# Kernel tuning notes

Measured on AMD Instinct MI355X. Metric: run time of the kernel, lower is better.

The kernel has to match this reference:

```python
import jax, jax.numpy as jnp
import numpy as np

B, T, I = 256, 1024, 64
P, E, NOUT = 256, 128, 64
K = 2
TEMP = 8.0
LN_EPS = 1e-5


def setup_inputs() -> dict:
    key = jax.random.key(0)
    ks = jax.random.split(key, 10)
    lim_in = 1.0 / np.sqrt(I)
    lim_e = 1.0 / np.sqrt(E)
    return {
        "x": jax.random.normal(ks[0], (B, T, I), dtype=jnp.float32),
        "pointer_init": jax.random.uniform(ks[1], (B,), dtype=jnp.float32) * P,
        "W_in": jax.random.uniform(ks[2], (E, I), minval=-lim_in, maxval=lim_in),
        "b_in": jax.random.uniform(ks[3], (E,), minval=-lim_in, maxval=lim_in),
        "ln_w": jnp.ones((E,), jnp.float32),
        "ln_b": jnp.zeros((E,), jnp.float32),
        "jump_dest": jax.random.uniform(ks[4], (P,), dtype=jnp.float32) * P,
        "Wg": jax.random.uniform(ks[5], (1, E), minval=-lim_e, maxval=lim_e),
        "bg": jax.random.uniform(ks[6], (1,), minval=-lim_e, maxval=lim_e),
        "context_strength": jnp.float32(0.2),
        "Wo": jax.random.uniform(ks[7], (NOUT, E), minval=-lim_e, maxval=lim_e),
        "bo": jax.random.uniform(ks[8], (NOUT,), minval=-lim_e, maxval=lim_e),
    }


def _layer_norm(h, w, b):
    mu = jnp.mean(h, axis=-1, keepdims=True)
    var = jnp.mean((h - mu) ** 2, axis=-1, keepdims=True)
    return (h - mu) * jax.lax.rsqrt(var + LN_EPS) * w + b


def reference(x, pointer_init, W_in, b_in, ln_w, ln_b, jump_dest, Wg, bg, context_strength, Wo, bo):
    Bsz = x.shape[0]
    nP = jump_dest.shape[0]
    offsets = jnp.arange(-K, K + 1, dtype=jnp.int32)  # [5]
    batch_idx = jnp.arange(Bsz)[:, None]               # [B,1]
    ctx_scale = jax.nn.sigmoid(context_strength)
    half = nP / 2.0

    def step(carry, x_t):
        mem, hid, ptr = carry                          # [B,P,E], [B,E], [B]
        emb = jnp.tanh(x_t @ W_in.T + b_in)            # [B,E]
        base = jnp.clip(jnp.floor(ptr).astype(jnp.int32), 0, nP - 1)
        idx = jnp.mod(base[:, None] + offsets[None, :], nP)  # [B,5]
        delta = jnp.mod(idx.astype(x_t.dtype) - ptr[:, None] + half, nP) - half
        w = jax.nn.softmax(-(delta ** 2) / TEMP, axis=1)     # [B,5]
        nbh = jnp.take_along_axis(mem, idx[:, :, None], axis=1)  # [B,5,E]
        ctx = jnp.sum(w[:, :, None] * nbh, axis=1)               # [B,E]
        su = jnp.tanh(emb + ctx_scale * ctx + hid)               # [B,E]
        hid_new = _layer_norm(su, ln_w, ln_b)
        mem_new = mem.at[batch_idx, idx].add(w[:, :, None] * su[:, None, :])
        cur = jnp.clip(ptr.astype(jnp.int32), 0, nP - 1)
        jt = jump_dest[cur]                                      # [B]
        jl = (su @ Wg.T + bg)[:, 0]                              # [B]
        probs = jax.nn.sigmoid(jl)
        sj = (probs > 0.5).astype(x_t.dtype) - jax.lax.stop_gradient(probs) + probs
        walk = jnp.mod(ptr + 1.0, nP)
        ptr_new = jnp.where(sj > 0.5, jt, walk)
        return (mem_new, hid_new, ptr_new), None

    mem0 = jnp.zeros((Bsz, nP, W_in.shape[0]), x.dtype)
    hid0 = jnp.zeros((Bsz, W_in.shape[0]), x.dtype)
    (mem, hid, ptr), _ = jax.lax.scan(step, (mem0, hid0, pointer_init), jnp.swapaxes(x, 0, 1))
    logits = hid @ Wo.T + bo
    return logits
```

## Files before the change

kernel.cpp:

```cpp
#include <hip/hip_runtime.h>
#include <math.h>

#define Bn    256
#define Tn    1024
#define In    64
#define Pn    256
#define En    128
#define NOUTn 64
#define LN_EPS 1e-5f

#define C1f 0.3606737602222409f
#define K1f 0.8824969025845955f
#define K2f 0.6065306597126334f

typedef float f32x2 __attribute__((ext_vector_type(2)));

__device__ __forceinline__ float tanh_fast(float x) {
    float e = __builtin_amdgcn_exp2f(x * 2.88539008177793f);
    return 1.0f - 2.0f * __builtin_amdgcn_rcpf(e + 1.0f);
}
__device__ __forceinline__ f32x2 tanh2(f32x2 x) {
    f32x2 e;
    e[0] = __builtin_amdgcn_exp2f(x[0] * 2.88539008177793f);
    e[1] = __builtin_amdgcn_exp2f(x[1] * 2.88539008177793f);
    f32x2 r;
    r[0] = __builtin_amdgcn_rcpf(e[0] + 1.0f);
    r[1] = __builtin_amdgcn_rcpf(e[1] + 1.0f);
    return 1.0f - 2.0f * r;
}

template<int CTRL, int RMASK>
__device__ __forceinline__ float dpp_add(float x) {
    return x + __int_as_float(__builtin_amdgcn_update_dpp(
        0, __float_as_int(x), CTRL, RMASK, 0xF, false));
}
__device__ __forceinline__ void wave_sum64_x3(float& x, float& y, float& z) {
#define LVL(C, R) x = dpp_add<C, R>(x); y = dpp_add<C, R>(y); z = dpp_add<C, R>(z);
    LVL(0x111, 0xF)
    LVL(0x112, 0xF)
    LVL(0x114, 0xF)
    LVL(0x118, 0xF)
    LVL(0x142, 0xA)
    LVL(0x143, 0xC)
#undef LVL
    x = __int_as_float(__builtin_amdgcn_readlane(__float_as_int(x), 63));
    y = __int_as_float(__builtin_amdgcn_readlane(__float_as_int(y), 63));
    z = __int_as_float(__builtin_amdgcn_readlane(__float_as_int(z), 63));
}

#define STAGE_FLOATS (3 * 16 * En)
#define LDSF_FLOATS  (Pn * En + Pn + STAGE_FLOATS)
#define LDSF_BYTES   (LDSF_FLOATS * 4)

__global__ __launch_bounds__(192, 1)
void fused2_kernel(const float* __restrict__ x,
                   const float* __restrict__ pointer_init,
                   const float* __restrict__ W_in, const float* __restrict__ b_in,
                   const float* __restrict__ ln_w, const float* __restrict__ ln_b,
                   const float* __restrict__ jump_dest,
                   const float* __restrict__ Wg,  const float* __restrict__ bg,
                   const float* __restrict__ cs_ptr,
                   const float* __restrict__ Wo,  const float* __restrict__ bo,
                   float* __restrict__ out) {
    extern __shared__ float lds[];
    float* mem = lds;
    float* jd  = lds + Pn * En;
    float* stg = lds + Pn * En + Pn;

    const int b   = blockIdx.x;
    const int tid = threadIdx.x;

    if (tid >= 64) {
        const int p    = tid - 64;
        const int tq   = p >> 5;
        const int eidx = p & 31;
        float be[4];
        #pragma unroll
        for (int j = 0; j < 4; ++j) be[j] = b_in[eidx + 32 * j];
        const float* xb = x + (size_t)b * Tn * In;

#define PRODUCE(K, BUF) {                                                     \
    const int t0 = (K) * 16 + tq * 4;                                         \
    const float4* xr = (const float4*)(xb + t0 * In);      \
    float acc[4][4];                                                          \
    _Pragma("unroll")                                                         \
    for (int tt = 0; tt < 4; ++tt)                                            \
        _Pragma("unroll")                                                     \
        for (int j = 0; j < 4; ++j) acc[tt][j] = 0.f;                         \
    _Pragma("unroll")                                                         \
    for (int i4 = 0; i4 < 16; ++i4) {                                         \
        float4 xv[4];                                                         \
        _Pragma("unroll")                                                     \
        for (int tt = 0; tt < 4; ++tt) xv[tt] = xr[tt * 16 + i4];             \
        float4 wf[4];                                                         \
        _Pragma("unroll")                                                     \
        for (int j = 0; j < 4; ++j)                                           \
            wf[j] = *(const float4*)(W_in + (eidx + 32 * j) * In + i4 * 4);   \
        _Pragma("unroll")                                                     \
        for (int tt = 0; tt < 4; ++tt)                                        \
            _Pragma("unroll")                                                 \
            for (int j = 0; j < 4; ++j) {                                     \
                acc[tt][j] += xv[tt].x * wf[j].x;                             \
                acc[tt][j] += xv[tt].y * wf[j].y;                             \
                acc[tt][j] += xv[tt].z * wf[j].z;                             \
                acc[tt][j] += xv[tt].w * wf[j].w;                             \
            }                                                                 \
    }                                                                         \
    float* sg = stg + (BUF) * 2048 + tq * 512;                                \
    _Pragma("unroll")                                                         \
    for (int j = 0; j < 4; ++j) {                                             \
        float4 o;                                                             \
        o.x = tanh_fast(acc[0][j] + be[j]);                                   \
        o.y = tanh_fast(acc[1][j] + be[j]);                                   \
        o.z = tanh_fast(acc[2][j] + be[j]);                                   \
        o.w = tanh_fast(acc[3][j] + be[j]);                                   \
        *(float4*)(sg + (eidx + 32 * j) * 4) = o;                             \
    }                                                                         \
}
        PRODUCE(0, 0)
        PRODUCE(1, 1)
        __syncthreads();
        int buf = 2;
        for (int k = 0; k < 64; ++k) {
            if (k + 2 < 64) {
                PRODUCE(k + 2, buf)
                buf = (buf == 2) ? 0 : buf + 1;
            }
            __syncthreads();
        }
#undef PRODUCE
        __syncthreads();
        return;
    }

    const int l = tid;

    float4* m4 = (float4*)mem;
    for (int i = l; i < Pn * En / 4; i += 64) m4[i] = make_float4(0.f, 0.f, 0.f, 0.f);
    for (int i = l; i < Pn; i += 64) jd[i] = jump_dest[i];

    const f32x2 lnw = {ln_w[l], ln_w[l + 64]};
    const f32x2 lnb = {ln_b[l], ln_b[l + 64]};
    const f32x2 wg  = {Wg[l],   Wg[l + 64]};
    const float bgs = bg[0];
    const float cs  = 1.0f / (1.0f + expf(-cs_ptr[0]));
    f32x2 hid = {0.f, 0.f};

    float* myb = mem + 2 * l;

    float jl      = 1.0f;
    float jt_cur  = pointer_init[b];
    float ptrW    = 0.f;
    int   baseW   = 0;
    float jtW_pre = 0.f;
    float z0 = 0.f, z1 = 0.f, z2 = 1.f, z3 = 0.f, z4 = 0.f, inv = 1.f;
    f32x2 wnb0 = {0,0}, wnb1 = {0,0}, wnb2 = {0,0}, wnb3 = {0,0}, wnb4 = {0,0};
    float *wp0 = myb, *wp1 = myb, *wp2 = myb, *wp3 = myb, *wp4 = myb;

    __syncthreads();

    const float* sa0 = stg + 4 * l;
    float4 A0 = *(const float4*)sa0;
    float4 A1 = *(const float4*)(sa0 + 256);

#define SSTEP(EC0, EC1) {                                                      \
    float ptr; int base;                                                       \
    f32x2 nb0, nb1, nb2, nb3, nb4;                                             \
    float *p0, *p1, *p2, *p3, *p4;                                             \
    float jt_nxt;                                                              \
    if (__builtin_amdgcn_readfirstlane(__float_as_int(jl)) > 0) {              \
                                     \
        ptr  = jt_cur;                                                         \
        base = (int)ptr; base = base > 255 ? 255 : base;                       \
        p0 = mem + (((base + 254) & 255) << 7) + 2 * l;                        \
        p1 = mem + (((base + 255) & 255) << 7) + 2 * l;                        \
        p2 = mem + (base << 7) + 2 * l;                                        \
        p3 = mem + (((base + 1) & 255) << 7) + 2 * l;                          \
        p4 = mem + (((base + 2) & 255) << 7) + 2 * l;                          \
        nb0 = *(f32x2*)p0; nb1 = *(f32x2*)p1; nb2 = *(f32x2*)p2;               \
        nb3 = *(f32x2*)p3; nb4 = *(f32x2*)p4;                                  \
        jt_nxt = jd[base];                                                     \
        const float frac = ptr - (float)base;                                  \
        const float r  = __builtin_amdgcn_exp2f(frac * C1f);                   \
        const float ri = __builtin_amdgcn_exp2f(-frac * C1f);                  \
        z0 = K2f * ri * ri; z1 = K1f * ri; z2 = 1.0f;                          \
        z3 = K1f * r;       z4 = K2f * r * r;                                  \
        inv = __builtin_amdgcn_rcpf(((z0 + z1) + (z2 + z3)) + z4);             \
    } else {                                                                   \
          \
        ptr = ptrW; base = baseW;                                              \
        nb0 = wnb0; nb1 = wnb1; nb2 = wnb2; nb3 = wnb3; nb4 = wnb4;            \
        p0 = wp0; p1 = wp1; p2 = wp2; p3 = wp3; p4 = wp4;                      \
        jt_nxt = jtW_pre;                                                      \
    }                                                                          \
    const f32x2 ctx = inv * (((nb0 * z0 + nb1 * z1) + (nb2 * z2 + nb3 * z3))   \
                             + nb4 * z4);                                      \
    f32x2 em; em[0] = (EC0); em[1] = (EC1);                                    \
    const f32x2 su = tanh2(em + cs * ctx + hid);                               \
    const f32x2 g  = su * inv;                                                 \
    const f32x2 m0v = nb0 + z0 * g, m1v = nb1 + z1 * g, m2v = nb2 + z2 * g,    \
                m3v = nb3 + z3 * g, m4v = nb4 + z4 * g;                        \
    *(f32x2*)p0 = m0v; *(f32x2*)p1 = m1v; *(f32x2*)p2 = m2v;                   \
    *(f32x2*)p3 = m3v; *(f32x2*)p4 = m4v;                                      \
     \
    baseW = (base + 1) & 255;                                                  \
    ptrW  = ptr + 1.0f; if (ptrW >= 256.0f) ptrW -= 256.0f;                    \
    wnb0 = m1v; wnb1 = m2v; wnb2 = m3v; wnb3 = m4v;                            \
    wp0 = p1; wp1 = p2; wp2 = p3; wp3 = p4;                                    \
    wp4 = mem + (((base + 3) & 255) << 7) + 2 * l;                             \
    wnb4 = *(f32x2*)wp4;                                                       \
    jtW_pre = jd[baseW];                                                       \
    jt_cur  = jt_nxt;                                                          \
                                                   \
    float s1 = su[0] + su[1];                                                  \
    const f32x2 sq = su * su;  float s2 = sq[0] + sq[1];                       \
    const f32x2 sg = su * wg;  float s3 = sg[0] + sg[1];                       \
    wave_sum64_x3(s1, s2, s3);                                                 \
    const float mu   = s1 * (1.0f / En);                                       \
    const float var  = s2 * (1.0f / En) - mu * mu;                             \
    const float rstd = __builtin_amdgcn_rsqf(var + LN_EPS);                    \
    hid = (su - mu) * rstd * lnw + lnb;                                        \
    jl  = s3 + bgs;                                                            \
}

    for (int k = 0; k < 64; ++k) {
        #pragma unroll
        for (int g = 0; g < 4; ++g) {
            const int tb  = k * 4 + g;
            int tbn = tb + 1; if (tbn > 255) tbn = 255;
            const float* sb = stg + ((tbn >> 2) % 3) * 2048 + (tbn & 3) * 512 + 4 * l;
            float4 B0 = *(const float4*)sb;
            float4 B1 = *(const float4*)(sb + 256);
            SSTEP(A0.x, A1.x)
            SSTEP(A0.y, A1.y)
            SSTEP(A0.z, A1.z)
            SSTEP(A0.w, A1.w)
            A0 = B0; A1 = B1;
        }
        __syncthreads();
    }
#undef SSTEP

    mem[l] = hid[0]; mem[64 + l] = hid[1];
    __syncthreads();
    const float4* w4 = (const float4*)(Wo + l * En);
    const float4* h4 = (const float4*)mem;
    float a0 = 0.f, a1 = 0.f, a2 = 0.f, a3 = 0.f;
    #pragma unroll
    for (int i = 0; i < En / 4; ++i) {
        float4 wv = w4[i]; float4 hv = h4[i];
        a0 += wv.x * hv.x; a1 += wv.y * hv.y; a2 += wv.z * hv.z; a3 += wv.w * hv.w;
    }
    out[b * NOUTn + l] = (a0 + a1) + (a2 + a3) + bo[l];
}

extern "C" void kernel_launch(void* const* d_in, const int* in_sizes, int n_in,
                              void* d_out, int out_size, void* d_ws, size_t ws_size,
                              hipStream_t stream) {
    const float* x            = (const float*)d_in[0];
    const float* pointer_init = (const float*)d_in[1];
    const float* W_in         = (const float*)d_in[2];
    const float* b_in         = (const float*)d_in[3];
    const float* ln_w         = (const float*)d_in[4];
    const float* ln_b         = (const float*)d_in[5];
    const float* jump_dest    = (const float*)d_in[6];
    const float* Wg           = (const float*)d_in[7];
    const float* bg           = (const float*)d_in[8];
    const float* cs           = (const float*)d_in[9];
    const float* Wo           = (const float*)d_in[10];
    const float* bo           = (const float*)d_in[11];
    float* out = (float*)d_out;
    (void)d_ws; (void)ws_size;

    (void)hipFuncSetAttribute((const void*)fused2_kernel,
                              hipFuncAttributeMaxDynamicSharedMemorySize, LDSF_BYTES);
    fused2_kernel<<<Bn, 192, LDSF_BYTES, stream>>>(
        x, pointer_init, W_in, b_in, ln_w, ln_b, jump_dest, Wg, bg, cs,
        Wo, bo, out);
}
```

Measured before the change: 472.8 us.

## Speculatively prefetch jump-target neighborhood each step and select branchlessly

Replaces the wave-uniform branch between the jump and walk paths with a branchless select. Both the walk-path neighborhood and the jump-target neighborhood (five memory rows, softmax weights, next jump destination) are prefetched one step ahead, so the serial recurrence no longer waits on LDS loads after a jump. The cost is extra LDS reads and exp/rcp work every step, even when no jump happens. The inner group loop is also no longer unrolled, likely to keep register pressure down.

```diff
diff --git a/kernel.cpp b/kernel.cpp
--- a/kernel.cpp
+++ b/kernel.cpp
@@ -148,53 +148,65 @@
 
     float* myb = mem + 2 * l;
 
-    float jl      = 1.0f;
-    float jt_cur  = pointer_init[b];
-    float ptrW    = 0.f;
-    int   baseW   = 0;
-    float jtW_pre = 0.f;
+    float jl = 1.0f;
     float z0 = 0.f, z1 = 0.f, z2 = 1.f, z3 = 0.f, z4 = 0.f, inv = 1.f;
+    float ptrW = 0.f; int baseW = 0; float jtW_pre = 0.f;
     f32x2 wnb0 = {0,0}, wnb1 = {0,0}, wnb2 = {0,0}, wnb3 = {0,0}, wnb4 = {0,0};
     float *wp0 = myb, *wp1 = myb, *wp2 = myb, *wp3 = myb, *wp4 = myb;
+    float jptr  = pointer_init[b];
+    int   jbase = (int)jptr; jbase = jbase > 255 ? 255 : jbase;
+    float jz0, jz1, jz2 = 1.f, jz3, jz4, jinv;
+    {
+        const float frac = jptr - (float)jbase;
+        const float r  = __builtin_amdgcn_exp2f(frac * C1f);
+        const float ri = __builtin_amdgcn_exp2f(-frac * C1f);
+        jz0 = K2f * ri * ri; jz1 = K1f * ri;
+        jz3 = K1f * r;       jz4 = K2f * r * r;
+        jinv = __builtin_amdgcn_rcpf(((jz0 + jz1) + (jz2 + jz3)) + jz4);
+    }
+    float *jp0 = mem + (((jbase + 254) & 255) << 7) + 2 * l;
+    float *jp1 = mem + (((jbase + 255) & 255) << 7) + 2 * l;
+    float *jp2 = mem + ((jbase) << 7) + 2 * l;
+    float *jp3 = mem + (((jbase + 1) & 255) << 7) + 2 * l;
+    float *jp4 = mem + (((jbase + 2) & 255) << 7) + 2 * l;
+    f32x2 jnb0, jnb1, jnb2, jnb3, jnb4;
+    float jjt;
 
     __syncthreads();
+
+    jnb0 = *(f32x2*)jp0; jnb1 = *(f32x2*)jp1; jnb2 = *(f32x2*)jp2;
+    jnb3 = *(f32x2*)jp3; jnb4 = *(f32x2*)jp4;
+    jjt  = jd[jbase];
 
     const float* sa0 = stg + 4 * l;
     float4 A0 = *(const float4*)sa0;
     float4 A1 = *(const float4*)(sa0 + 256);
 
 #define SSTEP(EC0, EC1) {                                                      \
-    float ptr; int base;                                                       \
-    f32x2 nb0, nb1, nb2, nb3, nb4;                                             \
-    float *p0, *p1, *p2, *p3, *p4;                                             \
-    float jt_nxt;                                                              \
-    if (__builtin_amdgcn_readfirstlane(__float_as_int(jl)) > 0) {              \
-                                     \
-        ptr  = jt_cur;                                                         \
-        base = (int)ptr; base = base > 255 ? 255 : base;                       \
-        p0 = mem + (((base + 254) & 255) << 7) + 2 * l;                        \
-        p1 = mem + (((base + 255) & 255) << 7) + 2 * l;                        \
-        p2 = mem + (base << 7) + 2 * l;                                        \
-        p3 = mem + (((base + 1) & 255) << 7) + 2 * l;                          \
-        p4 = mem + (((base + 2) & 255) << 7) + 2 * l;                          \
-        nb0 = *(f32x2*)p0; nb1 = *(f32x2*)p1; nb2 = *(f32x2*)p2;               \
-        nb3 = *(f32x2*)p3; nb4 = *(f32x2*)p4;                                  \
-        jt_nxt = jd[base];                                                     \
-        const float frac = ptr - (float)base;                                  \
-        const float r  = __builtin_amdgcn_exp2f(frac * C1f);                   \
-        const float ri = __builtin_amdgcn_exp2f(-frac * C1f);                  \
-        z0 = K2f * ri * ri; z1 = K1f * ri; z2 = 1.0f;                          \
-        z3 = K1f * r;       z4 = K2f * r * r;                                  \
-        inv = __builtin_amdgcn_rcpf(((z0 + z1) + (z2 + z3)) + z4);             \
-    } else {                                                                   \
-          \
-        ptr = ptrW; base = baseW;                                              \
-        nb0 = wnb0; nb1 = wnb1; nb2 = wnb2; nb3 = wnb3; nb4 = wnb4;            \
-        p0 = wp0; p1 = wp1; p2 = wp2; p3 = wp3; p4 = wp4;                      \
-        jt_nxt = jtW_pre;                                                      \
-    }                                                                          \
-    const f32x2 ctx = inv * (((nb0 * z0 + nb1 * z1) + (nb2 * z2 + nb3 * z3))   \
-                             + nb4 * z4);                                      \
+    const bool JMP = jl > 0.0f;                         \
+                  \
+    const f32x2 ctxW = inv  * (((wnb0 * z0  + wnb1 * z1 )                      \
+                              + (wnb2 * z2  + wnb3 * z3 )) + wnb4 * z4 );      \
+    const f32x2 ctxJ = jinv * (((jnb0 * jz0 + jnb1 * jz1)                      \
+                              + (jnb2 * jz2 + jnb3 * jz3)) + jnb4 * jz4);      \
+    f32x2 ctx; ctx[0] = JMP ? ctxJ[0] : ctxW[0];                               \
+               ctx[1] = JMP ? ctxJ[1] : ctxW[1];                               \
+               \
+    const float ptr  = JMP ? jptr  : ptrW;                                     \
+    const int   base = JMP ? jbase : baseW;                                    \
+    z0 = JMP ? jz0 : z0;  z1 = JMP ? jz1 : z1;                                 \
+    z3 = JMP ? jz3 : z3;  z4 = JMP ? jz4 : z4;                                 \
+    inv = JMP ? jinv : inv;                                                    \
+    const f32x2 nb0 = JMP ? jnb0 : wnb0;                                       \
+    const f32x2 nb1 = JMP ? jnb1 : wnb1;                                       \
+    const f32x2 nb2 = JMP ? jnb2 : wnb2;                                       \
+    const f32x2 nb3 = JMP ? jnb3 : wnb3;                                       \
+    const f32x2 nb4 = JMP ? jnb4 : wnb4;                                       \
+    float* p0 = JMP ? jp0 : wp0;  float* p1 = JMP ? jp1 : wp1;                 \
+    float* p2 = JMP ? jp2 : wp2;  float* p3 = JMP ? jp3 : wp3;                 \
+    float* p4 = JMP ? jp4 : wp4;                                               \
+    const float jt_n = JMP ? jjt : jtW_pre;                                    \
+                                      \
     f32x2 em; em[0] = (EC0); em[1] = (EC1);                                    \
     const f32x2 su = tanh2(em + cs * ctx + hid);                               \
     const f32x2 g  = su * inv;                                                 \
@@ -202,7 +214,7 @@
                 m3v = nb3 + z3 * g, m4v = nb4 + z4 * g;                        \
     *(f32x2*)p0 = m0v; *(f32x2*)p1 = m1v; *(f32x2*)p2 = m2v;                   \
     *(f32x2*)p3 = m3v; *(f32x2*)p4 = m4v;                                      \
-     \
+      \
     baseW = (base + 1) & 255;                                                  \
     ptrW  = ptr + 1.0f; if (ptrW >= 256.0f) ptrW -= 256.0f;                    \
     wnb0 = m1v; wnb1 = m2v; wnb2 = m3v; wnb3 = m4v;                            \
@@ -210,8 +222,26 @@
     wp4 = mem + (((base + 3) & 255) << 7) + 2 * l;                             \
     wnb4 = *(f32x2*)wp4;                                                       \
     jtW_pre = jd[baseW];                                                       \
-    jt_cur  = jt_nxt;                                                          \
-                                                   \
+                 \
+    jptr  = jt_n;                                                              \
+    jbase = (int)jptr; jbase = jbase > 255 ? 255 : jbase;                      \
+    {                                                                          \
+        const float frac = jptr - (float)jbase;                                \
+        const float r  = __builtin_amdgcn_exp2f(frac * C1f);                   \
+        const float ri = __builtin_amdgcn_exp2f(-frac * C1f);                  \
+        jz0 = K2f * ri * ri; jz1 = K1f * ri;                                   \
+        jz3 = K1f * r;       jz4 = K2f * r * r;                                \
+        jinv = __builtin_amdgcn_rcpf(((jz0 + jz1) + (jz2 + jz3)) + jz4);       \
+    }                                                                          \
+    jp0 = mem + (((jbase + 254) & 255) << 7) + 2 * l;                          \
+    jp1 = mem + (((jbase + 255) & 255) << 7) + 2 * l;                          \
+    jp2 = mem + ((jbase) << 7) + 2 * l;                                        \
+    jp3 = mem + (((jbase + 1) & 255) << 7) + 2 * l;                            \
+    jp4 = mem + (((jbase + 2) & 255) << 7) + 2 * l;                            \
+    jnb0 = *(f32x2*)jp0; jnb1 = *(f32x2*)jp1; jnb2 = *(f32x2*)jp2;             \
+    jnb3 = *(f32x2*)jp3; jnb4 = *(f32x2*)jp4;                                  \
+    jjt  = jd[jbase];                                                          \
+                                       \
     float s1 = su[0] + su[1];                                                  \
     const f32x2 sq = su * su;  float s2 = sq[0] + sq[1];                       \
     const f32x2 sg = su * wg;  float s3 = sg[0] + sg[1];                       \
@@ -224,9 +254,9 @@
 }
 
     for (int k = 0; k < 64; ++k) {
-        #pragma unroll
-        for (int g = 0; g < 4; ++g) {
-            const int tb  = k * 4 + g;
+        #pragma unroll 1
+        for (int gi = 0; gi < 4; ++gi) {
+            const int tb  = k * 4 + gi;
             int tbn = tb + 1; if (tbn > 255) tbn = 255;
             const float* sb = stg + ((tbn >> 2) % 3) * 2048 + (tbn & 3) * 512 + 4 * l;
             float4 B0 = *(const float4*)sb;
```

New measurement: 483.0 us. +2.2%, slower.

## Restructure recurrent step to precompute walk context before jump decision and raise wave priority

Applied to the files above, without the earlier changes.

Reorganizes each recurrence step so the walk-path context (shifted neighborhood plus the prefetched fifth row) is computed speculatively while the wave reduction runs. The jump branch, taken only when the gate fires, then overwrites the pointer, neighborhood and weights after the decision, instead of choosing between paths at the top of the next step. This shortens the serial dependency chain between the reduction and the next tanh. It also raises the compute wave's scheduling priority during the loop. The walk path always does some context arithmetic, and that work is thrown away whenever a jump is taken.

```diff
diff --git a/kernel.cpp b/kernel.cpp
--- a/kernel.cpp
+++ b/kernel.cpp
@@ -145,82 +145,88 @@
     const float bgs = bg[0];
     const float cs  = 1.0f / (1.0f + expf(-cs_ptr[0]));
     f32x2 hid = {0.f, 0.f};
-
-    float* myb = mem + 2 * l;
-
-    float jl      = 1.0f;
-    float jt_cur  = pointer_init[b];
-    float ptrW    = 0.f;
-    int   baseW   = 0;
-    float jtW_pre = 0.f;
-    float z0 = 0.f, z1 = 0.f, z2 = 1.f, z3 = 0.f, z4 = 0.f, inv = 1.f;
-    f32x2 wnb0 = {0,0}, wnb1 = {0,0}, wnb2 = {0,0}, wnb3 = {0,0}, wnb4 = {0,0};
-    float *wp0 = myb, *wp1 = myb, *wp2 = myb, *wp3 = myb, *wp4 = myb;
+    float jl;
+
+    float PTR = pointer_init[b];
+    int   it0 = (int)PTR;  int BASE = it0 > 255 ? 255 : it0;
+    float *P0 = mem + (((BASE + 254) & 255) << 7) + 2 * l;
+    float *P1 = mem + (((BASE + 255) & 255) << 7) + 2 * l;
+    float *P2 = mem + (BASE << 7) + 2 * l;
+    float *P3 = mem + (((BASE + 1) & 255) << 7) + 2 * l;
+    float *P4 = mem + (((BASE + 2) & 255) << 7) + 2 * l;
+    float Z0, Z1, Z2 = 1.0f, Z3, Z4, INV;
+    {
+        const float frac = PTR - (float)BASE;
+        const float r  = __builtin_amdgcn_exp2f(frac * C1f);
+        const float ri = __builtin_amdgcn_exp2f(-frac * C1f);
+        Z0 = K2f * ri * ri; Z1 = K1f * ri;
+        Z3 = K1f * r;       Z4 = K2f * r * r;
+        INV = __builtin_amdgcn_rcpf(((Z0 + Z1) + (Z2 + Z3)) + Z4);
+    }
 
     __syncthreads();
+    __builtin_amdgcn_s_setprio(1);
+
+    f32x2 NB0 = *(f32x2*)P0, NB1 = *(f32x2*)P1, NB2 = *(f32x2*)P2,
+          NB3 = *(f32x2*)P3, NB4 = *(f32x2*)P4;
+    f32x2 CTX = INV * (((NB0 * Z0 + NB1 * Z1) + (NB2 * Z2 + NB3 * Z3))
+                       + NB4 * Z4);
 
     const float* sa0 = stg + 4 * l;
     float4 A0 = *(const float4*)sa0;
     float4 A1 = *(const float4*)(sa0 + 256);
 
 #define SSTEP(EC0, EC1) {                                                      \
-    float ptr; int base;                                                       \
-    f32x2 nb0, nb1, nb2, nb3, nb4;                                             \
-    float *p0, *p1, *p2, *p3, *p4;                                             \
-    float jt_nxt;                                                              \
-    if (__builtin_amdgcn_readfirstlane(__float_as_int(jl)) > 0) {              \
-                                     \
-        ptr  = jt_cur;                                                         \
-        base = (int)ptr; base = base > 255 ? 255 : base;                       \
-        p0 = mem + (((base + 254) & 255) << 7) + 2 * l;                        \
-        p1 = mem + (((base + 255) & 255) << 7) + 2 * l;                        \
-        p2 = mem + (base << 7) + 2 * l;                                        \
-        p3 = mem + (((base + 1) & 255) << 7) + 2 * l;                          \
-        p4 = mem + (((base + 2) & 255) << 7) + 2 * l;                          \
-        nb0 = *(f32x2*)p0; nb1 = *(f32x2*)p1; nb2 = *(f32x2*)p2;               \
-        nb3 = *(f32x2*)p3; nb4 = *(f32x2*)p4;                                  \
-        jt_nxt = jd[base];                                                     \
-        const float frac = ptr - (float)base;                                  \
-        const float r  = __builtin_amdgcn_exp2f(frac * C1f);                   \
-        const float ri = __builtin_amdgcn_exp2f(-frac * C1f);                  \
-        z0 = K2f * ri * ri; z1 = K1f * ri; z2 = 1.0f;                          \
-        z3 = K1f * r;       z4 = K2f * r * r;                                  \
-        inv = __builtin_amdgcn_rcpf(((z0 + z1) + (z2 + z3)) + z4);             \
-    } else {                                                                   \
           \
-        ptr = ptrW; base = baseW;                                              \
-        nb0 = wnb0; nb1 = wnb1; nb2 = wnb2; nb3 = wnb3; nb4 = wnb4;            \
-        p0 = wp0; p1 = wp1; p2 = wp2; p3 = wp3; p4 = wp4;                      \
-        jt_nxt = jtW_pre;                                                      \
-    }                                                                          \
-    const f32x2 ctx = inv * (((nb0 * z0 + nb1 * z1) + (nb2 * z2 + nb3 * z3))   \
-                             + nb4 * z4);                                      \
+    float* wp4n = mem + (((BASE + 3) & 255) << 7) + 2 * l;                     \
+    const f32x2 wnb4n  = *(f32x2*)wp4n;                                        \
+    const float JTnext = jd[BASE];         \
     f32x2 em; em[0] = (EC0); em[1] = (EC1);                                    \
-    const f32x2 su = tanh2(em + cs * ctx + hid);                               \
-    const f32x2 g  = su * inv;                                                 \
-    const f32x2 m0v = nb0 + z0 * g, m1v = nb1 + z1 * g, m2v = nb2 + z2 * g,    \
-                m3v = nb3 + z3 * g, m4v = nb4 + z4 * g;                        \
-    *(f32x2*)p0 = m0v; *(f32x2*)p1 = m1v; *(f32x2*)p2 = m2v;                   \
-    *(f32x2*)p3 = m3v; *(f32x2*)p4 = m4v;                                      \
-     \
-    baseW = (base + 1) & 255;                                                  \
-    ptrW  = ptr + 1.0f; if (ptrW >= 256.0f) ptrW -= 256.0f;                    \
-    wnb0 = m1v; wnb1 = m2v; wnb2 = m3v; wnb3 = m4v;                            \
-    wp0 = p1; wp1 = p2; wp2 = p3; wp3 = p4;                                    \
-    wp4 = mem + (((base + 3) & 255) << 7) + 2 * l;                             \
-    wnb4 = *(f32x2*)wp4;                                                       \
-    jtW_pre = jd[baseW];                                                       \
-    jt_cur  = jt_nxt;                                                          \
-                                                   \
+    const f32x2 su = tanh2(em + cs * CTX + hid);                               \
+               \
     float s1 = su[0] + su[1];                                                  \
     const f32x2 sq = su * su;  float s2 = sq[0] + sq[1];                       \
     const f32x2 sg = su * wg;  float s3 = sg[0] + sg[1];                       \
     wave_sum64_x3(s1, s2, s3);                                                 \
+                                           \
+    const f32x2 g  = su * INV;                                                 \
+    const f32x2 m0v = NB0 + Z0 * g, m1v = NB1 + Z1 * g, m2v = NB2 + Z2 * g,    \
+                m3v = NB3 + Z3 * g, m4v = NB4 + Z4 * g;                        \
+    *(f32x2*)P0 = m0v; *(f32x2*)P1 = m1v; *(f32x2*)P2 = m2v;                   \
+    *(f32x2*)P3 = m3v; *(f32x2*)P4 = m4v;                                      \
+                     \
+    PTR = PTR + 1.0f; if (PTR >= 256.0f) PTR -= 256.0f;                        \
+    BASE = (BASE + 1) & 255;                                                   \
+    NB0 = m1v; NB1 = m2v; NB2 = m3v; NB3 = m4v; NB4 = wnb4n;                   \
+    P0 = P1; P1 = P2; P2 = P3; P3 = P4; P4 = wp4n;                             \
+    CTX = INV * (((NB0 * Z0 + NB1 * Z1) + (NB2 * Z2 + NB3 * Z3))               \
+                 + NB4 * Z4);                                                  \
+                                                                \
     const float mu   = s1 * (1.0f / En);                                       \
     const float var  = s2 * (1.0f / En) - mu * mu;                             \
     const float rstd = __builtin_amdgcn_rsqf(var + LN_EPS);                    \
     hid = (su - mu) * rstd * lnw + lnb;                                        \
     jl  = s3 + bgs;                                                            \
+                                  \
+    if (__builtin_amdgcn_readfirstlane(__float_as_int(jl)) > 0) {              \
+        PTR = JTnext;                                                          \
+        int ib = (int)PTR; BASE = ib > 255 ? 255 : ib;                         \
+        P0 = mem + (((BASE + 254) & 255) << 7) + 2 * l;                        \
+        P1 = mem + (((BASE + 255) & 255) << 7) + 2 * l;                        \
+        P2 = mem + (BASE << 7) + 2 * l;                                        \
+        P3 = mem + (((BASE + 1) & 255) << 7) + 2 * l;                          \
+        P4 = mem + (((BASE + 2) & 255) << 7) + 2 * l;                          \
+        NB0 = *(f32x2*)P0; NB1 = *(f32x2*)P1; NB2 = *(f32x2*)P2;               \
+        NB3 = *(f32x2*)P3; NB4 = *(f32x2*)P4;                                  \
+        const float frac = PTR - (float)BASE;                                  \
+        const float r  = __builtin_amdgcn_exp2f(frac * C1f);                   \
+        const float ri = __builtin_amdgcn_exp2f(-frac * C1f);                  \
+        Z0 = K2f * ri * ri; Z1 = K1f * ri; Z2 = 1.0f;                          \
+        Z3 = K1f * r;       Z4 = K2f * r * r;                                  \
+        INV = __builtin_amdgcn_rcpf(((Z0 + Z1) + (Z2 + Z3)) + Z4);             \
+        CTX = INV * (((NB0 * Z0 + NB1 * Z1) + (NB2 * Z2 + NB3 * Z3))           \
+                     + NB4 * Z4);                                              \
+    }                                                                          \
 }
 
     for (int k = 0; k < 64; ++k) {
@@ -241,6 +247,7 @@
     }
 #undef SSTEP
 
+    __builtin_amdgcn_s_setprio(0);
     mem[l] = hid[0]; mem[64 + l] = hid[1];
     __syncthreads();
     const float4* w4 = (const float4*)(Wo + l * En);
```

After: 471.8 us. About the same (-0.2%).
